# Kernel tuning notes

Measured on AMD Instinct MI355X. Metric: run time of the kernel, lower is better.

## Reference

```python
import jax, jax.numpy as jnp
import numpy as np

T, H = 1024, 2048          # tokens, hidden_size
E, K = 8, 4                # num_experts, top_k
I_E = 1408                 # moe_intermediate_size
I_S = 5632                 # shared_expert_intermediate_size


def setup_inputs() -> dict:
    key = jax.random.key(0)
    ks = jax.random.split(key, 7)
    s = 0.02
    return {
        "hidden_states": jax.random.normal(ks[0], (T, H), dtype=jnp.float32),
        "w_gate": jax.random.normal(ks[1], (H, E), dtype=jnp.float32) * s,
        "w_shared_gate": jax.random.normal(ks[2], (H, 1), dtype=jnp.float32) * s,
        "w_shared_gu": jax.random.normal(ks[3], (H, 2 * I_S), dtype=jnp.float32) * s,
        "w_shared_down": jax.random.normal(ks[4], (I_S, H), dtype=jnp.float32) * s,
        "w_exp_gu": jax.random.normal(ks[5], (E, H, 2 * I_E), dtype=jnp.float32) * s,
        "w_exp_down": jax.random.normal(ks[6], (E, I_E, H), dtype=jnp.float32) * s,
    }


def _silu_and_mul(gu):
    g, u = jnp.split(gu, 2, axis=-1)
    return jax.nn.silu(g) * u


def reference(hidden_states, w_gate, w_shared_gate, w_shared_gu, w_shared_down,
              w_exp_gu, w_exp_down):
    x = hidden_states  # [T, H]

    # ---- router: softmax -> top_k (norm_topk_prob=False, no renormalize) ----
    router_logits = x @ w_gate                       # [T, E]
    probs = jax.nn.softmax(router_logits, axis=-1)
    topw, topi = jax.lax.top_k(probs, K)             # [T, K] each
    # per-token combine weights over experts: [T, E]
    comb = jnp.sum(jax.nn.one_hot(topi, E, dtype=probs.dtype) * topw[..., None], axis=1)

    # ---- fused experts (dense-per-expert reference for grouped GEMM) ----
    gu = jnp.einsum('th,ehf->etf', x, w_exp_gu)      # [E, T, 2*I_E]
    act = _silu_and_mul(gu)                          # [E, T, I_E]
    out_e = jnp.einsum('etf,efh->eth', act, w_exp_down)  # [E, T, H]
    fused_out = jnp.einsum('eth,te->th', out_e, comb)    # [T, H]

    # ---- shared expert with sigmoid gate ----
    s_act = _silu_and_mul(x @ w_shared_gu)           # [T, I_S]
    shared_out = s_act @ w_shared_down               # [T, H]
    shared_out = jax.nn.sigmoid(x @ w_shared_gate) * shared_out

    return shared_out + fused_out
```

## Files before the change

kernel.cpp:

```cpp
#include <hip/hip_runtime.h>
#include <hip/hip_bf16.h>
#include <stdint.h>

#define T_TOK 1024
#define H_DIM 2048
#define NEXP 8
#define IED 1408
#define ISD 5632

typedef __attribute__((ext_vector_type(8))) short s16x8;
typedef __attribute__((ext_vector_type(8))) unsigned short u16x8;
typedef __attribute__((ext_vector_type(4))) float f32x4;

#define SWZ(r) (((r) ^ ((r) >> 2)) & 3)

__device__ __forceinline__ unsigned short f2bf(float f) {
  union { __hip_bfloat16 b; unsigned short u; } v;
  v.b = __float2bfloat16(f);
  return v.u;
}

__device__ __forceinline__ void gload16(const void* g, void* l) {
  __builtin_amdgcn_global_load_lds(
      (const __attribute__((address_space(1))) unsigned int*)g,
      (__attribute__((address_space(3))) unsigned int*)l, 16, 0, 0);
}

extern "C" __global__ void __launch_bounds__(256) k_router(
    const float* __restrict__ x, const float* __restrict__ wg,
    const float* __restrict__ wsg, unsigned short* __restrict__ xb,
    int* __restrict__ counts, int* __restrict__ tlist,
    float* __restrict__ wlist, float* __restrict__ gate_sig) {
  const int tid = threadIdx.x;
  const int bb = blockIdx.x;
#pragma unroll
  for (int it = 0; it < 8; it++) {
    int i = bb * 8192 + it * 1024 + tid * 4;
    float4 v = *(const float4*)(x + i);
    ushort4 o;
    o.x = f2bf(v.x); o.y = f2bf(v.y); o.z = f2bf(v.z); o.w = f2bf(v.w);
    *(ushort4*)(xb + i) = o;
  }
  const int lane = tid & 63;
  const int t = bb * 4 + (tid >> 6);
  const float* xr = x + (size_t)t * H_DIM;
  float acc[8];
#pragma unroll
  for (int e = 0; e < 8; e++) acc[e] = 0.f;
  float sg = 0.f;
  for (int h = lane; h < H_DIM; h += 64) {
    float xv = xr[h];
    float4 w0 = *(const float4*)(wg + h * 8);
    float4 w1 = *(const float4*)(wg + h * 8 + 4);
    acc[0] += xv * w0.x; acc[1] += xv * w0.y; acc[2] += xv * w0.z; acc[3] += xv * w0.w;
    acc[4] += xv * w1.x; acc[5] += xv * w1.y; acc[6] += xv * w1.z; acc[7] += xv * w1.w;
    sg += xv * wsg[h];
  }
#pragma unroll
  for (int d = 32; d >= 1; d >>= 1) {
#pragma unroll
    for (int e = 0; e < 8; e++) acc[e] += __shfl_xor(acc[e], d, 64);
    sg += __shfl_xor(sg, d, 64);
  }
  if (lane == 0) {
    float m = acc[0];
#pragma unroll
    for (int e = 1; e < 8; e++) m = fmaxf(m, acc[e]);
    float p[8], s = 0.f;
#pragma unroll
    for (int e = 0; e < 8; e++) { p[e] = __expf(acc[e] - m); s += p[e]; }
    float inv = 1.f / s;
    bool used[8];
#pragma unroll
    for (int e = 0; e < 8; e++) used[e] = false;
    for (int j = 0; j < 4; j++) {
      int be = 0; float bv = -1e30f;
#pragma unroll
      for (int e = 0; e < 8; e++)
        if (!used[e] && acc[e] > bv) { bv = acc[e]; be = e; }
      used[be] = true;
      int slot = atomicAdd(counts + be, 1);
      tlist[be * T_TOK + slot] = t;
      wlist[be * T_TOK + slot] = p[be] * inv;
    }
    gate_sig[t] = 1.f / (1.f + __expf(-sg));
  }
}

#define ISSUE_A(kk, AOFF)                                                 \
  do {                                                                    \
    gload16(asrc + (kk), adst + (AOFF));                                  \
    __builtin_amdgcn_sched_barrier(0);                                    \
  } while (0)

#define ISSUE_B(kk)                                                       \
  do {                                                                    \
    _Pragma("unroll") for (int j = 0; j < 8; j++)                         \
        RB[j] = Bh[(size_t)((kk) + bc * 8 + j) * (size_t)ldb];            \
    __builtin_amdgcn_sched_barrier(0);                                    \
  } while (0)

#define CVTB(BOFF)                                                        \
  do {                                                                    \
    u16x8 pk;                                                             \
    _Pragma("unroll") for (int j = 0; j < 8; j++) pk[j] = f2bf(RB[j]);    \
    *(u16x8*)(bwr + (BOFF)) = pk;                                         \
  } while (0)

#define COMPUTE(AOFF, BOFF)                                               \
  do {                                                                    \
    const unsigned short* ab = a_lds + (AOFF);                            \
    const unsigned short* bb2 = b_lds + (BOFF);                           \
    __builtin_amdgcn_s_setprio(1);                                        \
    {                                                                     \
      const int kc = lane >> 4;                                           \
      s16x8 afr[4];                                                       \
      _Pragma("unroll") for (int m = 0; m < 4; m++) {                     \
        int r = wm * 64 + m * 16 + (lane & 15);                           \
        afr[m] = *(const s16x8*)&ab[r * 32 + ((kc ^ SWZ(r)) * 8)];        \
      }                                                                   \
      _Pragma("unroll") for (int nf = 0; nf < 2; nf++) {                  \
        int rb_ = wn * 16 + nf * 64 + (lane & 15);                        \
        s16x8 bfr = *(const s16x8*)&bb2[rb_ * 32 + ((kc ^ SWZ(rb_)) * 8)]; \
        _Pragma("unroll") for (int m = 0; m < 4; m++)                     \
            acc[m][nf] = __builtin_amdgcn_mfma_f32_16x16x32_bf16(         \
                afr[m], bfr, acc[m][nf], 0, 0, 0);                        \
      }                                                                   \
    }                                                                     \
    __builtin_amdgcn_s_setprio(0);                                        \
  } while (0)

template <int DOWN>
__global__ void k_mm(
    const unsigned short* __restrict__ A_sh, const unsigned short* __restrict__ A_ex,
    const float* __restrict__ B_sh, const float* __restrict__ B_ex,
    unsigned short* __restrict__ act_sh, unsigned short* __restrict__ act_ex,
    float* __restrict__ out,
    const int* __restrict__ counts, const int* __restrict__ tlist,
    const float* __restrict__ wlist, const float* __restrict__ gate_sig) {
  const int tid = threadIdx.x;
  const int lane = tid & 63;
  const int wid = tid >> 6;
  const int wm = wid >> 2, wn = wid & 3;

  constexpr int SHBLK = DOWN ? 512 : 704;
  const int b0 = blockIdx.x;
  const bool ex = b0 >= SHBLK;
  const int b = ex ? b0 - SHBLK : b0;
  const int xcd = b & 7;
  const int j = b >> 3;
  const int mtile = j & 7;
  int e = 0, ntile = 0, z = 0;
  if constexpr (!DOWN) {
    if (!ex) ntile = xcd * 11 + (j >> 3);
    else { int p = xcd * 22 + (j >> 3); e = p & 7; ntile = p >> 3; }
  } else {
    if (!ex) { int p = xcd * 8 + (j >> 3); ntile = p >> 2; z = p & 3; }
    else { int p = xcd * 16 + (j >> 3); e = p & 7; ntile = p >> 3; }
  }

  int lda, ldb, IK = 0, kbeg = 0, count = T_TOK, nt;
  const unsigned short* A;
  const float* Bb0; const float* Bb1;
  const int* tlA = nullptr;
  const int* tlO = nullptr;
  const float* wl = nullptr;
  unsigned short* actout = nullptr;

  if constexpr (!DOWN) {
    lda = H_DIM; nt = 64;
    if (!ex) {
      ldb = 2 * ISD; IK = ISD; A = A_sh; actout = act_sh;
      Bb0 = B_sh + ntile * 64; Bb1 = B_sh + ISD + ntile * 64;
    } else {
      count = counts[e];
      if (mtile * 128 >= count) return;
      ldb = 2 * IED; IK = IED; A = A_sh;
      const float* Bw = B_ex + (size_t)e * H_DIM * (2 * IED);
      Bb0 = Bw + ntile * 64; Bb1 = Bw + IED + ntile * 64;
      tlA = tlist + e * T_TOK; wl = wlist + e * T_TOK;
      actout = act_ex + (size_t)e * T_TOK * IED;
    }
  } else {
    ldb = H_DIM; nt = 44;
    if (!ex) {
      lda = ISD; kbeg = z * 1408; A = A_sh;
      Bb0 = B_sh + ntile * 128; Bb1 = Bb0;
    } else {
      count = counts[e];
      if (mtile * 128 >= count) return;
      lda = IED; A = A_ex + (size_t)e * T_TOK * IED;
      Bb0 = B_ex + (size_t)e * IED * H_DIM + ntile * 128; Bb1 = Bb0;
      tlO = tlist + e * T_TOK;
    }
  }

  __shared__ unsigned short a_lds[2 * 4096];
  __shared__ unsigned short b_lds[2 * 4096];

  const unsigned short* asrc;
  unsigned short* adst;
  {
    int row = tid >> 2;
    int rowg = mtile * 128 + row;
    int arow = rowg;
    if (tlA) arow = tlA[rowg];
    asrc = A + (size_t)arow * lda + (((tid & 3) ^ SWZ(row)) * 8);
    adst = &a_lds[(tid >> 6) * 512];
  }

  const int bnn = tid & 127;
  const int bc = tid >> 7;
  const float* Bh;
  if constexpr (!DOWN) Bh = (bnn < 64) ? (Bb0 + bnn) : (Bb1 + (bnn - 64));
  else Bh = Bb0 + bnn;
  unsigned short* bwr = &b_lds[bnn * 32 + ((bc ^ SWZ(bnn)) * 8)];

  const f32x4 fzero = {0.f, 0.f, 0.f, 0.f};
  f32x4 acc[4][2];
#pragma unroll
  for (int m = 0; m < 4; m++)
#pragma unroll
    for (int n = 0; n < 2; n++) acc[m][n] = fzero;

  float RB[8];

  ISSUE_B(kbeg);
  ISSUE_A(kbeg, 0);
  CVTB(0);
  ISSUE_B(kbeg + 32);
  __builtin_amdgcn_sched_barrier(0);
  asm volatile("s_waitcnt vmcnt(8)" ::: "memory");
  asm volatile("s_waitcnt lgkmcnt(0)" ::: "memory");
  __builtin_amdgcn_s_barrier();
  __builtin_amdgcn_sched_barrier(0);

  for (int u = 0; u < nt; ++u) {
    const int cur = (u & 1) * 4096;
    const int nxt = cur ^ 4096;
    const int k0 = kbeg + u * 32;
    const bool haveN1 = (u + 1 < nt);
    const bool haveN2 = (u + 2 < nt);
    if (haveN1) {
      ISSUE_A(k0 + 32, nxt);
      CVTB(nxt);
      if (haveN2) ISSUE_B(k0 + 64);
    }
    COMPUTE(cur, cur);
    if (haveN1) {
      __builtin_amdgcn_sched_barrier(0);
      if (haveN2)
        asm volatile("s_waitcnt vmcnt(8)" ::: "memory");
      else
        asm volatile("s_waitcnt vmcnt(0)" ::: "memory");
      asm volatile("s_waitcnt lgkmcnt(0)" ::: "memory");
      __builtin_amdgcn_s_barrier();
      __builtin_amdgcn_sched_barrier(0);
    }
  }

  if constexpr (!DOWN) {
#pragma unroll
    for (int m = 0; m < 4; m++) {
#pragma unroll
      for (int i = 0; i < 4; i++) {
        int rowslot = mtile * 128 + wm * 64 + m * 16 + (lane >> 4) * 4 + i;
        float rsc = 1.f;
        if (wl) rsc = wl[rowslot];
        float g = acc[m][0][i];
        float u2 = acc[m][1][i];
        float sv = g / (1.f + __expf(-g)) * u2 * rsc;
        int col = ntile * 64 + wn * 16 + (lane & 15);
        actout[(size_t)rowslot * IK + col] = f2bf(sv);
      }
    }
  } else {
#pragma unroll
    for (int m = 0; m < 4; m++) {
#pragma unroll
      for (int i = 0; i < 4; i++) {
        int rowslot = mtile * 128 + wm * 64 + m * 16 + (lane >> 4) * 4 + i;
        int token = rowslot;
        if (tlO) token = tlO[rowslot];
        float sc = ex ? 1.f : gate_sig[token];
        float* orow = out + (size_t)token * H_DIM + ntile * 128 + wn * 16 + (lane & 15);
#pragma unroll
        for (int nf = 0; nf < 2; nf++)
          atomicAdd(orow + nf * 64, acc[m][nf][i] * sc);
      }
    }
  }
}

extern "C" void kernel_launch(void* const* d_in, const int* in_sizes, int n_in,
                              void* d_out, int out_size, void* d_ws, size_t ws_size,
                              hipStream_t stream) {
  (void)in_sizes; (void)n_in; (void)out_size; (void)ws_size;
  const float* x    = (const float*)d_in[0];
  const float* wg   = (const float*)d_in[1];
  const float* wsg  = (const float*)d_in[2];
  const float* wsgu = (const float*)d_in[3];
  const float* wsd  = (const float*)d_in[4];
  const float* wegu = (const float*)d_in[5];
  const float* wed  = (const float*)d_in[6];
  float* out = (float*)d_out;

  char* ws = (char*)d_ws;
  unsigned short* xb   = (unsigned short*)ws;
  unsigned short* acts = (unsigned short*)(ws + (4u << 20));
  unsigned short* acte = (unsigned short*)(ws + (4u << 20) + 11534336u);
  char* ctrl = ws + (4u << 20) + 11534336u + 23068672u;
  int* counts    = (int*)ctrl;
  int* tlist     = (int*)(ctrl + 256);
  float* wlist   = (float*)(ctrl + 256 + 32768);
  float* gate_sig = (float*)(ctrl + 256 + 65536);

  hipMemsetAsync(d_out, 0, (size_t)T_TOK * H_DIM * 4, stream);
  hipMemsetAsync(ctrl, 0, 256 + 65536, stream);

  k_router<<<dim3(256), dim3(256), 0, stream>>>(x, wg, wsg, xb, counts, tlist, wlist, gate_sig);
  k_mm<0><<<dim3(2112), dim3(512), 0, stream>>>(xb, xb, wsgu, wegu, acts, acte, nullptr,
                                                counts, tlist, wlist, gate_sig);
  k_mm<1><<<dim3(1536), dim3(512), 0, stream>>>(acts, acte, wsd, wed, nullptr, nullptr, out,
                                                counts, tlist, wlist, gate_sig);
}
```

Before: 472.0 us.

## Triple-buffer A tiles in LDS to prefetch two k-steps ahead

The A operand's LDS staging grows from double to triple buffering. A global-to-LDS loads are now issued two k-iterations ahead instead of one, and the buffers rotate each step. The explicit vmcnt waits are removed and each phase barrier waits only on lgkmcnt. Completion of the A loads is left to the implicit in-order wait that the compiler inserts before converting the B registers. The aim is to hide more global-load latency, at the cost of 8 KB more LDS per block, which may lower occupancy, and a subtler load-completion dependency.

Result: no change. 477.5 us (+1.1%).

```diff
diff --git a/kernel.cpp b/kernel.cpp
--- a/kernel.cpp
+++ b/kernel.cpp
@@ -130,6 +130,14 @@
     __builtin_amdgcn_s_setprio(0);                                        \
   } while (0)
 
+#define PHASE_BAR()                                                       \
+  do {                                                                    \
+    __builtin_amdgcn_sched_barrier(0);                                    \
+    asm volatile("s_waitcnt lgkmcnt(0)" ::: "memory");                    \
+    __builtin_amdgcn_s_barrier();                                         \
+    __builtin_amdgcn_sched_barrier(0);                                    \
+  } while (0)
+
 template <int DOWN>
 __global__ void k_mm(
     const unsigned short* __restrict__ A_sh, const unsigned short* __restrict__ A_ex,
@@ -144,6 +152,7 @@
   const int wm = wid >> 2, wn = wid & 3;
 
   constexpr int SHBLK = DOWN ? 512 : 704;
+  constexpr int nt = DOWN ? 44 : 64;
   const int b0 = blockIdx.x;
   const bool ex = b0 >= SHBLK;
   const int b = ex ? b0 - SHBLK : b0;
@@ -159,7 +168,7 @@
     else { int p = xcd * 16 + (j >> 3); e = p & 7; ntile = p >> 3; }
   }
 
-  int lda, ldb, IK = 0, kbeg = 0, count = T_TOK, nt;
+  int lda, ldb, IK = 0, kbeg = 0, count = T_TOK;
   const unsigned short* A;
   const float* Bb0; const float* Bb1;
   const int* tlA = nullptr;
@@ -168,7 +177,7 @@
   unsigned short* actout = nullptr;
 
   if constexpr (!DOWN) {
-    lda = H_DIM; nt = 64;
+    lda = H_DIM;
     if (!ex) {
       ldb = 2 * ISD; IK = ISD; A = A_sh; actout = act_sh;
       Bb0 = B_sh + ntile * 64; Bb1 = B_sh + ISD + ntile * 64;
@@ -182,7 +191,7 @@
       actout = act_ex + (size_t)e * T_TOK * IED;
     }
   } else {
-    ldb = H_DIM; nt = 44;
+    ldb = H_DIM;
     if (!ex) {
       lda = ISD; kbeg = z * 1408; A = A_sh;
       Bb0 = B_sh + ntile * 128; Bb1 = Bb0;
@@ -195,7 +204,7 @@
     }
   }
 
-  __shared__ unsigned short a_lds[2 * 4096];
+  __shared__ unsigned short a_lds[3 * 4096];
   __shared__ unsigned short b_lds[2 * 4096];
 
   const unsigned short* asrc;
@@ -224,39 +233,25 @@
     for (int n = 0; n < 2; n++) acc[m][n] = fzero;
 
   float RB[8];
-
+  int a0 = 0, a1 = 4096, a2 = 8192;
+  int bcur = 0;
+
+  ISSUE_A(kbeg, 0);
   ISSUE_B(kbeg);
-  ISSUE_A(kbeg, 0);
+  ISSUE_A(kbeg + 32, 4096);
   CVTB(0);
   ISSUE_B(kbeg + 32);
-  __builtin_amdgcn_sched_barrier(0);
-  asm volatile("s_waitcnt vmcnt(8)" ::: "memory");
-  asm volatile("s_waitcnt lgkmcnt(0)" ::: "memory");
-  __builtin_amdgcn_s_barrier();
-  __builtin_amdgcn_sched_barrier(0);
+  PHASE_BAR();
 
   for (int u = 0; u < nt; ++u) {
-    const int cur = (u & 1) * 4096;
-    const int nxt = cur ^ 4096;
     const int k0 = kbeg + u * 32;
-    const bool haveN1 = (u + 1 < nt);
-    const bool haveN2 = (u + 2 < nt);
-    if (haveN1) {
-      ISSUE_A(k0 + 32, nxt);
-      CVTB(nxt);
-      if (haveN2) ISSUE_B(k0 + 64);
-    }
-    COMPUTE(cur, cur);
-    if (haveN1) {
-      __builtin_amdgcn_sched_barrier(0);
-      if (haveN2)
-        asm volatile("s_waitcnt vmcnt(8)" ::: "memory");
-      else
-        asm volatile("s_waitcnt vmcnt(0)" ::: "memory");
-      asm volatile("s_waitcnt lgkmcnt(0)" ::: "memory");
-      __builtin_amdgcn_s_barrier();
-      __builtin_amdgcn_sched_barrier(0);
-    }
+    if (u + 2 < nt) ISSUE_A(k0 + 64, a2);
+    if (u + 1 < nt) CVTB(bcur ^ 4096);
+    if (u + 2 < nt) ISSUE_B(k0 + 64);
+    COMPUTE(a0, bcur);
+    if (u + 1 < nt) PHASE_BAR();
+    int t_ = a0; a0 = a1; a1 = a2; a2 = t_;
+    bcur ^= 4096;
   }
 
   if constexpr (!DOWN) {
```
